# Kernel tuning notes

Measured on AMD Instinct MI355X. Metric: run time of the kernel, lower is better.

## Reference

```python
import jax, jax.numpy as jnp
import numpy as np

G, S, DG, HN, HE, L, F = 64, 160, 128, 128, 16, 2, 16


def _rn(k, shape, scale=0.05):
    return jax.random.normal(k, shape, dtype=jnp.float32) * scale


def setup_inputs() -> dict:
    ks = jax.random.split(jax.random.key(0), 26)
    return {
        "gene_codes": jax.random.normal(ks[0], (G, DG), dtype=jnp.float32),
        "node_entry_w": _rn(ks[1], (HN, DG)), "node_entry_b": _rn(ks[2], (HN,)),
        "node_wih0": _rn(ks[3], (4 * HN, 1)), "node_wih": _rn(ks[4], (L - 1, 4 * HN, HN)),
        "node_whh": _rn(ks[5], (L, 4 * HN, HN)), "node_bih": _rn(ks[6], (L, 4 * HN)), "node_bhh": _rn(ks[7], (L, 4 * HN)),
        "node_exit_w": _rn(ks[8], (32, HN)), "node_exit_b": _rn(ks[9], (32,)),
        "edge_entry_w": _rn(ks[10], (HE, 32)), "edge_entry_b": _rn(ks[11], (HE,)),
        "edge_wih0": _rn(ks[12], (4 * HE, 1)), "edge_wih": _rn(ks[13], (L - 1, 4 * HE, HE)),
        "edge_whh": _rn(ks[14], (L, 4 * HE, HE)), "edge_bih": _rn(ks[15], (L, 4 * HE)), "edge_bhh": _rn(ks[16], (L, 4 * HE)),
        "ee1_w": _rn(ks[17], (8, HE)), "ee1_b": _rn(ks[18], (8,)),
        "ee2_w": _rn(ks[19], (2, 8)), "ee2_b": _rn(ks[20], (2,)),
        "ef1_w": _rn(ks[21], (8, HE)), "ef1_b": _rn(ks[22], (8,)),
        "ef2_w": _rn(ks[23], (2 * F, 8)), "ef2_b": _rn(ks[24], (2 * F,)),
        "graphs_size": S,
    }


def _lstm_zero_input(h0, wih0, wih, whh, bih, bhh, steps):
    # Multi-layer PyTorch-style LSTM (gate order i,f,g,o) whose input sequence is all-zeros
    # of feature size 1; h0 is replicated across layers (as in the original .repeat).
    nl = whh.shape[0]
    h = jnp.stack([h0] * nl)
    c = jnp.zeros_like(h)
    zero_in = jnp.zeros((h0.shape[0], 1), h0.dtype)

    def step(carry, _):
        h, c = carry
        hs, cs = [], []
        inp = zero_in
        for l in range(nl):
            w_in = wih0 if l == 0 else wih[l - 1]
            gates = inp @ w_in.T + h[l] @ whh[l].T + bih[l] + bhh[l]
            i, f, g, o = jnp.split(gates, 4, axis=-1)
            cn = jax.nn.sigmoid(f) * c[l] + jax.nn.sigmoid(i) * jnp.tanh(g)
            hn = jax.nn.sigmoid(o) * jnp.tanh(cn)
            hs.append(hn); cs.append(cn)
            inp = hn
        return (jnp.stack(hs), jnp.stack(cs)), hs[-1]

    _, outs = jax.lax.scan(step, (h, c), None, length=steps)
    return outs  # [steps, B, H] top-layer hiddens


def reference(gene_codes, node_entry_w, node_entry_b, node_wih0, node_wih, node_whh, node_bih, node_bhh, node_exit_w, node_exit_b, edge_entry_w, edge_entry_b, edge_wih0, edge_wih, edge_whh, edge_bih, edge_bhh, ee1_w, ee1_b, ee2_w, ee2_b, ef1_w, ef1_b, ef2_w, ef2_b, graphs_size):
    s_len = int(graphs_size)
    g_n = gene_codes.shape[0]
    n_max = s_len + 1
    m = s_len * g_n  # total node steps == number of edge sequences
    fdim = ef2_w.shape[0] // 2

    # node RNN over zero inputs, h0 from gene codes
    h0n = jax.nn.relu(gene_codes @ node_entry_w.T + node_entry_b)
    node_out = _lstm_zero_input(h0n, node_wih0, node_wih, node_whh, node_bih, node_bhh, s_len)  # [S,G,HN]
    # uniform graph sizes: torch's flipped packed data == reversed step-major layout,
    # flat index k -> (step = S-1-k//G, graph = k%G)
    node_flat = jnp.flip(node_out, axis=0).reshape(m, -1)

    # edge RNN: one sequence per node step; zero inputs, so full-length run gives
    # identical hiddens at every valid packed step
    h0e = jax.nn.relu(jax.nn.relu(node_flat @ node_exit_w.T + node_exit_b) @ edge_entry_w.T + edge_entry_b)
    eh = _lstm_zero_input(h0e, edge_wih0, edge_wih, edge_whh, edge_bih, edge_bhh, s_len)  # [S,M,HE]

    e = jax.nn.sigmoid(jax.nn.relu(eh @ ee1_w.T + ee1_b) @ ee2_w.T + ee2_b)          # [S,M,2]
    f = (jax.nn.relu(eh @ ef1_w.T + ef1_b) @ ef2_w.T + ef2_b).reshape(s_len, m, 2, fdim)

    # ragged index construction: edge sequence k has row = edges_size[k] = S - k//G,
    # graph id = k%G, valid steps s < row, column = s
    k = jnp.arange(m)
    gid = k % g_n
    row = s_len - k // g_n
    s = jnp.arange(s_len)[:, None]
    mask = (s < row[None, :]).reshape(-1)
    gid2 = jnp.broadcast_to(gid[None, :], (s_len, m)).reshape(-1)
    row2 = jnp.broadcast_to(row[None, :], (s_len, m)).reshape(-1)
    col2 = jnp.broadcast_to(s, (s_len, m)).reshape(-1)

    el = jnp.where(mask, e[..., 0].reshape(-1), 0.0)
    eu = jnp.where(mask, e[..., 1].reshape(-1), 0.0)
    exist = jnp.zeros((g_n, n_max, n_max), gene_codes.dtype)
    exist = exist.at[gid2, row2, col2].add(el).at[gid2, col2, row2].add(eu)

    fl = jnp.where(mask[:, None], f[:, :, 0, :].reshape(-1, fdim), 0.0)
    fu = jnp.where(mask[:, None], f[:, :, 1, :].reshape(-1, fdim), 0.0)
    feat = jnp.zeros((g_n, n_max, n_max, fdim), gene_codes.dtype)
    feat = feat.at[gid2, row2, col2].add(fl).at[gid2, col2, row2].add(fu)
    return exist, feat
```

## Files before the change

### kernel.cpp

```cpp
#include <hip/hip_runtime.h>


typedef __attribute__((ext_vector_type(8))) short short8;
typedef __attribute__((ext_vector_type(4))) short short4v;
typedef __attribute__((ext_vector_type(4))) float floatx4;
typedef _Float16 half2v __attribute__((ext_vector_type(2)));

#define NG 64
#define NMAX 161

__device__ __forceinline__ float sgm(float x) {
  return __builtin_amdgcn_rcpf(1.0f + __expf(-x));
}
__device__ __forceinline__ float tanhf_(float x) {
  return 2.0f * __builtin_amdgcn_rcpf(1.0f + __expf(-2.0f * x)) - 1.0f;
}
__device__ __forceinline__ unsigned short f2b(float x) {
  union { float f; unsigned u; } v; v.f = x;
  unsigned r = v.u + 0x7fffu + ((v.u >> 16) & 1u);
  return (unsigned short)(r >> 16);
}
__device__ __forceinline__ float b2f(unsigned short h) {
  union { unsigned u; float f; } v; v.u = ((unsigned)h) << 16; return v.f;
}
__device__ __forceinline__ half2v pkh(float a, float b) {
  return __builtin_bit_cast(half2v, __builtin_amdgcn_cvt_pkrtz(a, b));
}

#define RORF(x, N) __builtin_bit_cast(float, __builtin_amdgcn_update_dpp(      \
    __builtin_bit_cast(int, (x)), __builtin_bit_cast(int, (x)),                \
    0x120 | (N), 0xF, 0xF, false))

__device__ __forceinline__ void rotpack(float h, half2v* out) {
  const float r1  = RORF(h, 1),  r2  = RORF(h, 2),  r3  = RORF(h, 3);
  const float r4  = RORF(h, 4),  r5  = RORF(h, 5),  r6  = RORF(h, 6);
  const float r7  = RORF(h, 7),  r8  = RORF(h, 8),  r9  = RORF(h, 9);
  const float r10 = RORF(h, 10), r11 = RORF(h, 11), r12 = RORF(h, 12);
  const float r13 = RORF(h, 13), r14 = RORF(h, 14), r15 = RORF(h, 15);
  out[0] = pkh(h,   r1);
  out[1] = pkh(r2,  r3);
  out[2] = pkh(r4,  r5);
  out[3] = pkh(r6,  r7);
  out[4] = pkh(r8,  r9);
  out[5] = pkh(r10, r11);
  out[6] = pkh(r12, r13);
  out[7] = pkh(r14, r15);
}

__global__ __launch_bounds__(512) void node_l0(
    const float* __restrict__ gene,
    const float* __restrict__ entw,
    const float* __restrict__ entb,
    const float* __restrict__ nwhh,
    const float* __restrict__ nbih,
    const float* __restrict__ nbhh,
    unsigned short* __restrict__ h0w,
    unsigned short* __restrict__ hinit)
{
  const int tid  = threadIdx.x;
  const int wv   = tid >> 6;
  const int lane = tid & 63;
  const int lo   = lane & 15;
  const int hi   = lane >> 4;
  const int u    = (wv << 4) | lo;
  const int nb   = blockIdx.x;

  __shared__ __align__(16) unsigned short hA0[2][16][136];

  short8 B0[4][4];
#pragma unroll
  for (int t = 0; t < 4; ++t) {
    const int n = t * 128 + u;
#pragma unroll
    for (int ks = 0; ks < 4; ++ks) {
      const float* src = nwhh + n * 128 + ks * 32 + hi * 8;
      short8 bfr;
#pragma unroll
      for (int jj = 0; jj < 8; ++jj) bfr[jj] = (short)f2b(src[jj]);
      B0[t][ks] = bfr;
    }
  }

  const float bi0 = nbih[u]       + nbhh[u];
  const float bf0 = nbih[128 + u] + nbhh[128 + u];
  const float bg0 = nbih[256 + u] + nbhh[256 + u];
  const float bo0 = nbih[384 + u] + nbhh[384 + u];

  {
    const int q  = tid >> 5;
    const int u4 = (tid & 31) * 4;
    const float* gc = gene + (nb * 16 + q) * 128;
    float acc[4] = { entb[u4], entb[u4 + 1], entb[u4 + 2], entb[u4 + 3] };
    for (int qq = 0; qq < 32; ++qq) {
      const float4 gv = *(const float4*)&gc[qq * 4];
#pragma unroll
      for (int r = 0; r < 4; ++r) {
        const float4 wv2 = *(const float4*)&entw[(u4 + r) * 128 + qq * 4];
        acc[r] += gv.x * wv2.x + gv.y * wv2.y + gv.z * wv2.z + gv.w * wv2.w;
      }
    }
#pragma unroll
    for (int r = 0; r < 4; ++r) {
      const unsigned short hb = f2b(fmaxf(acc[r], 0.0f));
      hA0[0][q][u4 + r] = hb;
      hinit[(size_t)(nb * 16 + q) * 128 + u4 + r] = hb;
    }
  }

  float c0[4] = {0.f, 0.f, 0.f, 0.f};
  __syncthreads();

  for (int t = 0; t < 160; ++t) {
    const int rb = t & 1, wb = rb ^ 1;
    floatx4 a0 = {bi0, bi0, bi0, bi0};
    floatx4 a1 = {bf0, bf0, bf0, bf0};
    floatx4 a2 = {bg0, bg0, bg0, bg0};
    floatx4 a3 = {bo0, bo0, bo0, bo0};
    const unsigned short* ar = &hA0[rb][lo][hi * 8];
#pragma unroll
    for (int ks = 0; ks < 4; ++ks) {
      const short8 afr = *(const short8*)(ar + ks * 32);
      a0 = __builtin_amdgcn_mfma_f32_16x16x32_bf16(afr, B0[0][ks], a0, 0, 0, 0);
      a1 = __builtin_amdgcn_mfma_f32_16x16x32_bf16(afr, B0[1][ks], a1, 0, 0, 0);
      a2 = __builtin_amdgcn_mfma_f32_16x16x32_bf16(afr, B0[2][ks], a2, 0, 0, 0);
      a3 = __builtin_amdgcn_mfma_f32_16x16x32_bf16(afr, B0[3][ks], a3, 0, 0, 0);
    }
    const size_t obase = (size_t)(t * 64 + nb * 16) * 128;
#pragma unroll
    for (int r = 0; r < 4; ++r) {
      const float iv = sgm(a0[r]);
      const float fv = sgm(a1[r]);
      const float gv = tanhf_(a2[r]);
      const float ov = sgm(a3[r]);
      const float cn = fv * c0[r] + iv * gv;
      c0[r] = cn;
      const unsigned short hb = f2b(ov * tanhf_(cn));
      const int q = hi * 4 + r;
      hA0[wb][q][u] = hb;
      h0w[obase + (size_t)q * 128 + u] = hb;
    }
    __syncthreads();
  }
}

__global__ __launch_bounds__(256) void xgemm(
    const unsigned short* __restrict__ h0w,
    const float* __restrict__ nwih,
    unsigned short* __restrict__ X3)
{
  const int tid = threadIdx.x;
  const int wv  = tid >> 6;
  const int lane = tid & 63;
  const int lo  = lane & 15;
  const int hi  = lane >> 4;
  const int bt  = blockIdx.x;
  const int bn  = blockIdx.y;

  __shared__ __align__(16) unsigned short s_b[128][136];

  for (int i = tid; i < 128 * 32; i += 256) {
    const int nc = i >> 5, k4 = (i & 31) * 4;
    const float4 w = *(const float4*)&nwih[(size_t)(bn * 128 + nc) * 128 + k4];
    s_b[nc][k4]     = f2b(w.x);
    s_b[nc][k4 + 1] = f2b(w.y);
    s_b[nc][k4 + 2] = f2b(w.z);
    s_b[nc][k4 + 3] = f2b(w.w);
  }
  __syncthreads();

  floatx4 acc[8];
#pragma unroll
  for (int nt = 0; nt < 8; ++nt) acc[nt] = (floatx4){0.f, 0.f, 0.f, 0.f};

  const unsigned short* arow = h0w + (size_t)(bt * 64 + wv * 16 + lo) * 128 + hi * 8;
#pragma unroll
  for (int ks = 0; ks < 4; ++ks) {
    const short8 afr = *(const short8*)(arow + ks * 32);
#pragma unroll
    for (int nt = 0; nt < 8; ++nt) {
      const short8 bfr = *(const short8*)&s_b[nt * 16 + lo][ks * 32 + hi * 8];
      acc[nt] = __builtin_amdgcn_mfma_f32_16x16x32_bf16(afr, bfr, acc[nt], 0, 0, 0);
    }
  }

#pragma unroll
  for (int nt = 0; nt < 8; ++nt) {
    const size_t base3 = ((((size_t)wv * 160 + bt) * 512) + bn * 128 + nt * 16 + lo) * 16 + hi * 4;
    short4v xv;
#pragma unroll
    for (int r = 0; r < 4; ++r) xv[r] = (short)f2b(acc[nt][r]);
    *(short4v*)&X3[base3] = xv;
  }
}

__global__ __launch_bounds__(512) void node_l1(
    const unsigned short* __restrict__ hinit,
    const unsigned short* __restrict__ X3,
    const float* __restrict__ nwhh,
    const float* __restrict__ nbih,
    const float* __restrict__ nbhh,
    unsigned short* __restrict__ nout)
{
  const int tid  = threadIdx.x;
  const int wv   = tid >> 6;
  const int lane = tid & 63;
  const int lo   = lane & 15;
  const int hi   = lane >> 4;
  const int u    = (wv << 4) | lo;
  const int nb   = blockIdx.x;

  __shared__ __align__(16) unsigned short hA1[2][16][136];

  short8 B1[4][4];
#pragma unroll
  for (int t = 0; t < 4; ++t) {
    const int n = t * 128 + u;
#pragma unroll
    for (int ks = 0; ks < 4; ++ks) {
      const float* src = nwhh + 512 * 128 + n * 128 + ks * 32 + hi * 8;
      short8 bfr;
#pragma unroll
      for (int jj = 0; jj < 8; ++jj) bfr[jj] = (short)f2b(src[jj]);
      B1[t][ks] = bfr;
    }
  }

  const float bi1 = nbih[512 + u]       + nbhh[512 + u];
  const float bf1 = nbih[512 + 128 + u] + nbhh[512 + 128 + u];
  const float bg1 = nbih[512 + 256 + u] + nbhh[512 + 256 + u];
  const float bo1 = nbih[512 + 384 + u] + nbhh[512 + 384 + u];

  {
    const int q  = tid >> 5;
    const int u4 = (tid & 31) * 4;
    const short4v hv = *(const short4v*)&hinit[(size_t)(nb * 16 + q) * 128 + u4];
    *(short4v*)&hA1[0][q][u4] = hv;
  }

  float c1[4] = {0.f, 0.f, 0.f, 0.f};

  const size_t xstep = 512 * 16;
  const unsigned short* xb = X3 + ((size_t)nb * 160) * xstep + (size_t)u * 16 + hi * 4;
  short4v x0 = *(const short4v*)(xb);
  short4v x1 = *(const short4v*)(xb + 128 * 16);
  short4v x2 = *(const short4v*)(xb + 256 * 16);
  short4v x3 = *(const short4v*)(xb + 384 * 16);
  __syncthreads();

  for (int t = 0; t < 160; ++t) {
    const int rb = t & 1, wb = rb ^ 1;

    floatx4 a0 = {bi1, bi1, bi1, bi1};
    floatx4 a1 = {bf1, bf1, bf1, bf1};
    floatx4 a2 = {bg1, bg1, bg1, bg1};
    floatx4 a3 = {bo1, bo1, bo1, bo1};
    const unsigned short* ar = &hA1[rb][lo][hi * 8];
#pragma unroll
    for (int ks = 0; ks < 4; ++ks) {
      const short8 afr = *(const short8*)(ar + ks * 32);
      a0 = __builtin_amdgcn_mfma_f32_16x16x32_bf16(afr, B1[0][ks], a0, 0, 0, 0);
      a1 = __builtin_amdgcn_mfma_f32_16x16x32_bf16(afr, B1[1][ks], a1, 0, 0, 0);
      a2 = __builtin_amdgcn_mfma_f32_16x16x32_bf16(afr, B1[2][ks], a2, 0, 0, 0);
      a3 = __builtin_amdgcn_mfma_f32_16x16x32_bf16(afr, B1[3][ks], a3, 0, 0, 0);
    }

    const short4v cx0 = x0, cx1 = x1, cx2 = x2, cx3 = x3;
    if (t + 1 < 160) {
      const unsigned short* xn = xb + (size_t)(t + 1) * xstep;
      x0 = *(const short4v*)(xn);
      x1 = *(const short4v*)(xn + 128 * 16);
      x2 = *(const short4v*)(xn + 256 * 16);
      x3 = *(const short4v*)(xn + 384 * 16);
    }

    const size_t obase = (size_t)((159 - t) * 64 + nb * 16) * 128;
#pragma unroll
    for (int r = 0; r < 4; ++r) {
      const float iv = sgm(a0[r] + b2f((unsigned short)cx0[r]));
      const float fv = sgm(a1[r] + b2f((unsigned short)cx1[r]));
      const float gv = tanhf_(a2[r] + b2f((unsigned short)cx2[r]));
      const float ov = sgm(a3[r] + b2f((unsigned short)cx3[r]));
      const float cn = fv * c1[r] + iv * gv;
      c1[r] = cn;
      const unsigned short hb = f2b(ov * tanhf_(cn));
      const int q = hi * 4 + r;
      hA1[wb][q][u] = hb;
      nout[obase + (size_t)q * 128 + u] = hb;
    }
    __syncthreads();
  }
}

__global__ __launch_bounds__(256, 1) void edge_kernel(
    const unsigned short* __restrict__ nflat,
    const float* __restrict__ exw, const float* __restrict__ exb,
    const float* __restrict__ enw, const float* __restrict__ enb,
    const float* __restrict__ ewih,
    const float* __restrict__ ewhh,
    const float* __restrict__ ebih, const float* __restrict__ ebhh,
    const float* __restrict__ ee1w, const float* __restrict__ ee1b,
    const float* __restrict__ ee2w, const float* __restrict__ ee2b,
    const float* __restrict__ ef1w, const float* __restrict__ ef1b,
    const float* __restrict__ ef2w, const float* __restrict__ ef2b,
    float* __restrict__ out)
{
  const int tid = threadIdx.x;
  const int sg  = tid >> 4;
  const int u   = tid & 15;
  const int b   = blockIdx.x;

  const int row = b >> 8, r = b & 255;
  const int bb  = (row == 1) ? (511 - r) : ((row << 8) + r);
  const int kbase = bb * 16;
  const int jrow  = 160 - (bb >> 2);
  const int gid   = (kbase & 63) + sg;

  __shared__ __align__(16) float s_nf[16][132];
  __shared__ float s_w0s[64][17];
  __shared__ float s_was[64][17];
  __shared__ float s_wbs[64][17];
  __shared__ float s_wh[16][17];
  __shared__ float s_ef2[32][10];
  __shared__ __align__(16) float s_ee2[16];
  __shared__ __align__(16) float t1b[16][12];
  __shared__ __align__(16) float t2b[16][12];
  __shared__ __align__(16) float x32[16][36];

  for (int i = tid; i < 16 * 128; i += 256)
    s_nf[i >> 7][i & 127] = b2f(nflat[(size_t)(kbase + (i >> 7)) * 128 + (i & 127)]);
  for (int i = tid; i < 64 * 16; i += 256) {
    s_w0s[i >> 4][i & 15] = ewhh[i];
    s_was[i >> 4][i & 15] = ewih[i];
    s_wbs[i >> 4][i & 15] = ewhh[1024 + i];
  }
  for (int i = tid; i < 8 * 16; i += 256) {
    s_wh[i >> 4][i & 15]       = ee1w[i];
    s_wh[8 + (i >> 4)][i & 15] = ef1w[i];
  }
  for (int i = tid; i < 32 * 8; i += 256) s_ef2[i >> 3][i & 7] = ef2w[i];
  if (tid < 16) s_ee2[tid] = ee2w[tid];

  if (b < NG) {
    for (int d = tid; d < NMAX; d += 256) {
      out[(size_t)b * (NMAX * NMAX) + (size_t)d * NMAX + d] = 0.0f;
      float* fb = out + (size_t)NG * NMAX * NMAX
                + ((size_t)b * NMAX * NMAX + (size_t)d * NMAX + d) * 16;
#pragma unroll
      for (int q = 0; q < 16; ++q) fb[q] = 0.0f;
    }
  }

  const float be0i = ebih[u]      + ebhh[u];
  const float be0f = ebih[16 + u] + ebhh[16 + u];
  const float be0g = ebih[32 + u] + ebhh[32 + u];
  const float be0o = ebih[48 + u] + ebhh[48 + u];
  const float be1i = ebih[64 + u]      + ebhh[64 + u];
  const float be1f = ebih[64 + 16 + u] + ebhh[64 + 16 + u];
  const float be1g = ebih[64 + 32 + u] + ebhh[64 + 32 + u];
  const float be1o = ebih[64 + 48 + u] + ebhh[64 + 48 + u];
  const float hbias = (u < 8) ? ee1b[u] : ef1b[u - 8];
  const float f2bl = ef2b[u], f2bu = ef2b[16 + u];
  const float e2bias = (u < 2) ? ee2b[u] : 0.0f;

  __syncthreads();

  half2v W0h[4][8], WAh[4][8], WBh[4][8], WHh[8];
#pragma unroll
  for (int g = 0; g < 4; ++g) {
    const int rw = g * 16 + u;
#pragma unroll
    for (int j = 0; j < 8; ++j) {
      const int v0 = (u + 2 * j) & 15, v1 = (u + 2 * j + 1) & 15;
      W0h[g][j] = pkh(s_w0s[rw][v0], s_w0s[rw][v1]);
      WAh[g][j] = pkh(s_was[rw][v0], s_was[rw][v1]);
      WBh[g][j] = pkh(s_wbs[rw][v0], s_wbs[rw][v1]);
    }
  }
#pragma unroll
  for (int j = 0; j < 8; ++j) {
    const int v0 = (u + 2 * j) & 15, v1 = (u + 2 * j + 1) & 15;
    WHh[j] = pkh(s_wh[u][v0], s_wh[u][v1]);
  }

  {
    float acc0 = exb[u], acc1 = exb[16 + u];
    const float* w0p = exw + u * 128;
    const float* w1p = exw + (16 + u) * 128;
    for (int qq = 0; qq < 32; ++qq) {
      const float4 nv  = *(const float4*)&s_nf[sg][qq * 4];
      const float4 w0v = *(const float4*)&w0p[qq * 4];
      const float4 w1v = *(const float4*)&w1p[qq * 4];
      acc0 += nv.x * w0v.x + nv.y * w0v.y + nv.z * w0v.z + nv.w * w0v.w;
      acc1 += nv.x * w1v.x + nv.y * w1v.y + nv.z * w1v.z + nv.w * w1v.w;
    }
    x32[sg][u] = fmaxf(acc0, 0.0f);
    x32[sg][16 + u] = fmaxf(acc1, 0.0f);
  }
  __builtin_amdgcn_wave_barrier();
  float c0 = 0.0f, c1 = 0.0f;
  half2v h20[8], h21[8];
  {
    float acc = enb[u];
    const float* ewp = enw + u * 32;
#pragma unroll
    for (int qq = 0; qq < 8; ++qq) {
      const float4 xv  = *(const float4*)&x32[sg][qq * 4];
      const float4 wv2 = *(const float4*)&ewp[qq * 4];
      acc += xv.x * wv2.x + xv.y * wv2.y + xv.z * wv2.z + xv.w * wv2.w;
    }
    const float h0e = fmaxf(acc, 0.0f);
    rotpack(h0e, h20);
#pragma unroll
    for (int j = 0; j < 8; ++j) h21[j] = h20[j];
  }

  float* exi = out + (size_t)gid * (NMAX * NMAX);
  float* fea = out + (size_t)NG * NMAX * NMAX + (size_t)gid * (NMAX * NMAX) * 16;
  const int jN = jrow * NMAX;

  for (int s = 0; s <= jrow; ++s) {
    const bool doStep = (s < jrow);
    const bool doHead = (s > 0);

    float a0, a1, a2, a3;
    if (doStep) {
      a0 = be0i; a1 = be0f; a2 = be0g; a3 = be0o;
#pragma unroll
      for (int j = 0; j < 8; ++j) {
        a0 = __builtin_amdgcn_fdot2(h20[j], W0h[0][j], a0, false);
        a1 = __builtin_amdgcn_fdot2(h20[j], W0h[1][j], a1, false);
        a2 = __builtin_amdgcn_fdot2(h20[j], W0h[2][j], a2, false);
        a3 = __builtin_amdgcn_fdot2(h20[j], W0h[3][j], a3, false);
      }
    }

    if (doHead) {
      __builtin_amdgcn_wave_barrier();
      const int sm = s - 1;
      const float2 ta0 = *(const float2*)&t2b[sg][0];
      const float2 ta1 = *(const float2*)&t2b[sg][2];
      const float2 ta2 = *(const float2*)&t2b[sg][4];
      const float2 ta3 = *(const float2*)&t2b[sg][6];
      const float2 wl0 = *(const float2*)&s_ef2[u][0];
      const float2 wl1 = *(const float2*)&s_ef2[u][2];
      const float2 wl2 = *(const float2*)&s_ef2[u][4];
      const float2 wl3 = *(const float2*)&s_ef2[u][6];
      const float2 wu0 = *(const float2*)&s_ef2[16 + u][0];
      const float2 wu1 = *(const float2*)&s_ef2[16 + u][2];
      const float2 wu2 = *(const float2*)&s_ef2[16 + u][4];
      const float2 wu3 = *(const float2*)&s_ef2[16 + u][6];
      const float fl = f2bl
          + ta0.x * wl0.x + ta0.y * wl0.y + ta1.x * wl1.x + ta1.y * wl1.y
          + ta2.x * wl2.x + ta2.y * wl2.y + ta3.x * wl3.x + ta3.y * wl3.y;
      const float fu = f2bu
          + ta0.x * wu0.x + ta0.y * wu0.y + ta1.x * wu1.x + ta1.y * wu1.y
          + ta2.x * wu2.x + ta2.y * wu2.y + ta3.x * wu3.x + ta3.y * wu3.y;
      fea[((size_t)jN + sm) * 16 + u] = fl;
      fea[((size_t)sm * NMAX + jrow) * 16 + u] = fu;
      if (u < 2) {
        const float4 t1a = *(const float4*)&t1b[sg][0];
        const float4 t1c = *(const float4*)&t1b[sg][4];
        const float4 we0 = *(const float4*)&s_ee2[u * 8];
        const float4 we1 = *(const float4*)&s_ee2[u * 8 + 4];
        float e = e2bias
            + t1a.x * we0.x + t1a.y * we0.y + t1a.z * we0.z + t1a.w * we0.w
            + t1c.x * we1.x + t1c.y * we1.y + t1c.z * we1.z + t1c.w * we1.w;
        const size_t idx = (u == 0) ? ((size_t)jN + sm)
                                    : ((size_t)sm * NMAX + jrow);
        exi[idx] = sgm(e);
      }
    }

    if (doStep) {
      {
        const float iv = sgm(a0), fv = sgm(a1), gv = tanhf_(a2), ov = sgm(a3);
        c0 = fv * c0 + iv * gv;
        rotpack(ov * tanhf_(c0), h20);
      }
      float b0 = be1i, b1 = be1f, b2 = be1g, b3 = be1o;
#pragma unroll
      for (int j = 0; j < 8; ++j) {
        b0 = __builtin_amdgcn_fdot2(h20[j], WAh[0][j], b0, false);
        b1 = __builtin_amdgcn_fdot2(h20[j], WAh[1][j], b1, false);
        b2 = __builtin_amdgcn_fdot2(h20[j], WAh[2][j], b2, false);
        b3 = __builtin_amdgcn_fdot2(h20[j], WAh[3][j], b3, false);
      }
#pragma unroll
      for (int j = 0; j < 8; ++j) {
        b0 = __builtin_amdgcn_fdot2(h21[j], WBh[0][j], b0, false);
        b1 = __builtin_amdgcn_fdot2(h21[j], WBh[1][j], b1, false);
        b2 = __builtin_amdgcn_fdot2(h21[j], WBh[2][j], b2, false);
        b3 = __builtin_amdgcn_fdot2(h21[j], WBh[3][j], b3, false);
      }
      {
        const float iv = sgm(b0), fv = sgm(b1), gv = tanhf_(b2), ov = sgm(b3);
        c1 = fv * c1 + iv * gv;
        rotpack(ov * tanhf_(c1), h21);
      }
      {
        float th = hbias;
#pragma unroll
        for (int j = 0; j < 8; ++j)
          th = __builtin_amdgcn_fdot2(h21[j], WHh[j], th, false);
        th = fmaxf(th, 0.0f);
        if (u < 8) t1b[sg][u] = th; else t2b[sg][u - 8] = th;
      }
      __builtin_amdgcn_wave_barrier();
    }
  }
}

extern "C" void kernel_launch(void* const* d_in, const int* in_sizes, int n_in,
                              void* d_out, int out_size, void* d_ws, size_t ws_size,
                              hipStream_t stream) {
  (void)in_sizes; (void)n_in; (void)out_size; (void)ws_size;
  const float* gene = (const float*)d_in[0];
  const float* entw = (const float*)d_in[1];
  const float* entb = (const float*)d_in[2];
  const float* nwih = (const float*)d_in[4];
  const float* nwhh = (const float*)d_in[5];
  const float* nbih = (const float*)d_in[6];
  const float* nbhh = (const float*)d_in[7];
  const float* exw  = (const float*)d_in[8];
  const float* exb  = (const float*)d_in[9];
  const float* enw  = (const float*)d_in[10];
  const float* enb  = (const float*)d_in[11];
  const float* ewih = (const float*)d_in[13];
  const float* ewhh = (const float*)d_in[14];
  const float* ebih = (const float*)d_in[15];
  const float* ebhh = (const float*)d_in[16];
  const float* ee1w = (const float*)d_in[17];
  const float* ee1b = (const float*)d_in[18];
  const float* ee2w = (const float*)d_in[19];
  const float* ee2b = (const float*)d_in[20];
  const float* ef1w = (const float*)d_in[21];
  const float* ef1b = (const float*)d_in[22];
  const float* ef2w = (const float*)d_in[23];
  const float* ef2b = (const float*)d_in[24];

  char* ws = (char*)d_ws;
  unsigned short* nflat = (unsigned short*)(ws);
  unsigned short* h0w   = (unsigned short*)(ws + 2621440);
  unsigned short* hinit = (unsigned short*)(ws + 5242880);
  unsigned short* X3    = (unsigned short*)(ws + 5259264);

  node_l0<<<4, 512, 0, stream>>>(gene, entw, entb, nwhh, nbih, nbhh, h0w, hinit);
  xgemm<<<dim3(160, 4), 256, 0, stream>>>(h0w, nwih, X3);
  node_l1<<<4, 512, 0, stream>>>(hinit, X3, nwhh, nbih, nbhh, nflat);
  edge_kernel<<<640, 256, 0, stream>>>(nflat, exw, exb, enw, enb, ewih, ewhh,
                                       ebih, ebhh, ee1w, ee1b, ee2w, ee2b,
                                       ef1w, ef1b, ef2w, ef2b, (float*)d_out);
}
```

Before: 501.6 us.

## Fuse node LSTM layers and input GEMM into one flag-pipelined persistent kernel

Replaces the three sequential node kernels (layer-0 recurrence, input-projection GEMM, layer-1 recurrence) with one 12-block launch. Blocks take three roles and hand work along through per-timestep global atomic flags, so the layer-1 recurrence can run one step behind layer 0 instead of waiting for it to finish. The initial hidden state is recomputed in the layer-1 blocks rather than stored and reloaded, and outputs use nontemporal stores. It adds spin-wait and fence latency on every step and relies on all 12 blocks being resident at the same time, and the layer-1 loop loses its one-step X prefetch.

```diff
diff --git a/kernel.cpp b/kernel.cpp
--- a/kernel.cpp
+++ b/kernel.cpp
@@ -47,247 +47,255 @@
   out[7] = pkh(r14, r15);
 }
 
-__global__ __launch_bounds__(512) void node_l0(
+__global__ __launch_bounds__(512) void node_fused(
     const float* __restrict__ gene,
     const float* __restrict__ entw,
     const float* __restrict__ entb,
+    const float* __restrict__ nwih,
     const float* __restrict__ nwhh,
     const float* __restrict__ nbih,
     const float* __restrict__ nbhh,
     unsigned short* __restrict__ h0w,
-    unsigned short* __restrict__ hinit)
+    unsigned short* __restrict__ X3,
+    unsigned short* __restrict__ nflat,
+    int* __restrict__ flag0, int* __restrict__ flag1)
 {
+  __shared__ __align__(16) unsigned short hA[2][16][136];
+  __shared__ __align__(16) unsigned short s_b[128][136];
+
   const int tid  = threadIdx.x;
+  const int role = blockIdx.x >> 2;
+  const int rb4  = blockIdx.x & 3;
   const int wv   = tid >> 6;
   const int lane = tid & 63;
   const int lo   = lane & 15;
   const int hi   = lane >> 4;
-  const int u    = (wv << 4) | lo;
-  const int nb   = blockIdx.x;
-
-  __shared__ __align__(16) unsigned short hA0[2][16][136];
-
-  short8 B0[4][4];
-#pragma unroll
-  for (int t = 0; t < 4; ++t) {
-    const int n = t * 128 + u;
-#pragma unroll
-    for (int ks = 0; ks < 4; ++ks) {
-      const float* src = nwhh + n * 128 + ks * 32 + hi * 8;
-      short8 bfr;
-#pragma unroll
-      for (int jj = 0; jj < 8; ++jj) bfr[jj] = (short)f2b(src[jj]);
-      B0[t][ks] = bfr;
-    }
-  }
-
-  const float bi0 = nbih[u]       + nbhh[u];
-  const float bf0 = nbih[128 + u] + nbhh[128 + u];
-  const float bg0 = nbih[256 + u] + nbhh[256 + u];
-  const float bo0 = nbih[384 + u] + nbhh[384 + u];
-
-  {
-    const int q  = tid >> 5;
-    const int u4 = (tid & 31) * 4;
-    const float* gc = gene + (nb * 16 + q) * 128;
-    float acc[4] = { entb[u4], entb[u4 + 1], entb[u4 + 2], entb[u4 + 3] };
-    for (int qq = 0; qq < 32; ++qq) {
-      const float4 gv = *(const float4*)&gc[qq * 4];
+
+  if (role == 0) {
+    const int nb = rb4;
+    const int u  = (wv << 4) | lo;
+
+    short8 B0[4][4];
+#pragma unroll
+    for (int t = 0; t < 4; ++t) {
+      const int n = t * 128 + u;
+#pragma unroll
+      for (int ks = 0; ks < 4; ++ks) {
+        const float* src = nwhh + n * 128 + ks * 32 + hi * 8;
+        short8 bfr;
+#pragma unroll
+        for (int jj = 0; jj < 8; ++jj) bfr[jj] = (short)f2b(src[jj]);
+        B0[t][ks] = bfr;
+      }
+    }
+    const float bi0 = nbih[u]       + nbhh[u];
+    const float bf0 = nbih[128 + u] + nbhh[128 + u];
+    const float bg0 = nbih[256 + u] + nbhh[256 + u];
+    const float bo0 = nbih[384 + u] + nbhh[384 + u];
+
+    {
+      const int q  = tid >> 5;
+      const int u4 = (tid & 31) * 4;
+      const float* gc = gene + (nb * 16 + q) * 128;
+      float acc[4] = { entb[u4], entb[u4 + 1], entb[u4 + 2], entb[u4 + 3] };
+      for (int qq = 0; qq < 32; ++qq) {
+        const float4 gv = *(const float4*)&gc[qq * 4];
+#pragma unroll
+        for (int r = 0; r < 4; ++r) {
+          const float4 wv2 = *(const float4*)&entw[(u4 + r) * 128 + qq * 4];
+          acc[r] += gv.x * wv2.x + gv.y * wv2.y + gv.z * wv2.z + gv.w * wv2.w;
+        }
+      }
+#pragma unroll
+      for (int r = 0; r < 4; ++r)
+        hA[0][q][u4 + r] = f2b(fmaxf(acc[r], 0.0f));
+    }
+
+    float c0[4] = {0.f, 0.f, 0.f, 0.f};
+    for (int t = 0; t < 160; ++t) {
+      __syncthreads();
+      if (t > 0 && tid == 0) {
+        __threadfence();
+        __hip_atomic_fetch_add(&flag0[t - 1], 1, __ATOMIC_RELEASE,
+                               __HIP_MEMORY_SCOPE_AGENT);
+      }
+      const int rb = t & 1, wb = rb ^ 1;
+      floatx4 a0 = {bi0, bi0, bi0, bi0};
+      floatx4 a1 = {bf0, bf0, bf0, bf0};
+      floatx4 a2 = {bg0, bg0, bg0, bg0};
+      floatx4 a3 = {bo0, bo0, bo0, bo0};
+      const unsigned short* ar = &hA[rb][lo][hi * 8];
+#pragma unroll
+      for (int ks = 0; ks < 4; ++ks) {
+        const short8 afr = *(const short8*)(ar + ks * 32);
+        a0 = __builtin_amdgcn_mfma_f32_16x16x32_bf16(afr, B0[0][ks], a0, 0, 0, 0);
+        a1 = __builtin_amdgcn_mfma_f32_16x16x32_bf16(afr, B0[1][ks], a1, 0, 0, 0);
+        a2 = __builtin_amdgcn_mfma_f32_16x16x32_bf16(afr, B0[2][ks], a2, 0, 0, 0);
+        a3 = __builtin_amdgcn_mfma_f32_16x16x32_bf16(afr, B0[3][ks], a3, 0, 0, 0);
+      }
+      const size_t obase = (size_t)(t * 64 + nb * 16) * 128;
 #pragma unroll
       for (int r = 0; r < 4; ++r) {
-        const float4 wv2 = *(const float4*)&entw[(u4 + r) * 128 + qq * 4];
-        acc[r] += gv.x * wv2.x + gv.y * wv2.y + gv.z * wv2.z + gv.w * wv2.w;
-      }
-    }
-#pragma unroll
-    for (int r = 0; r < 4; ++r) {
-      const unsigned short hb = f2b(fmaxf(acc[r], 0.0f));
-      hA0[0][q][u4 + r] = hb;
-      hinit[(size_t)(nb * 16 + q) * 128 + u4 + r] = hb;
-    }
-  }
-
-  float c0[4] = {0.f, 0.f, 0.f, 0.f};
-  __syncthreads();
-
-  for (int t = 0; t < 160; ++t) {
-    const int rb = t & 1, wb = rb ^ 1;
-    floatx4 a0 = {bi0, bi0, bi0, bi0};
-    floatx4 a1 = {bf0, bf0, bf0, bf0};
-    floatx4 a2 = {bg0, bg0, bg0, bg0};
-    floatx4 a3 = {bo0, bo0, bo0, bo0};
-    const unsigned short* ar = &hA0[rb][lo][hi * 8];
-#pragma unroll
-    for (int ks = 0; ks < 4; ++ks) {
-      const short8 afr = *(const short8*)(ar + ks * 32);
-      a0 = __builtin_amdgcn_mfma_f32_16x16x32_bf16(afr, B0[0][ks], a0, 0, 0, 0);
-      a1 = __builtin_amdgcn_mfma_f32_16x16x32_bf16(afr, B0[1][ks], a1, 0, 0, 0);
-      a2 = __builtin_amdgcn_mfma_f32_16x16x32_bf16(afr, B0[2][ks], a2, 0, 0, 0);
-      a3 = __builtin_amdgcn_mfma_f32_16x16x32_bf16(afr, B0[3][ks], a3, 0, 0, 0);
-    }
-    const size_t obase = (size_t)(t * 64 + nb * 16) * 128;
-#pragma unroll
-    for (int r = 0; r < 4; ++r) {
-      const float iv = sgm(a0[r]);
-      const float fv = sgm(a1[r]);
-      const float gv = tanhf_(a2[r]);
-      const float ov = sgm(a3[r]);
-      const float cn = fv * c0[r] + iv * gv;
-      c0[r] = cn;
-      const unsigned short hb = f2b(ov * tanhf_(cn));
-      const int q = hi * 4 + r;
-      hA0[wb][q][u] = hb;
-      h0w[obase + (size_t)q * 128 + u] = hb;
+        const float iv = sgm(a0[r]);
+        const float fv = sgm(a1[r]);
+        const float gv = tanhf_(a2[r]);
+        const float ov = sgm(a3[r]);
+        const float cn = fv * c0[r] + iv * gv;
+        c0[r] = cn;
+        const unsigned short hb = f2b(ov * tanhf_(cn));
+        const int q = hi * 4 + r;
+        hA[wb][q][u] = hb;
+        __builtin_nontemporal_store(hb, &h0w[obase + (size_t)q * 128 + u]);
+      }
     }
     __syncthreads();
-  }
-}
-
-__global__ __launch_bounds__(256) void xgemm(
-    const unsigned short* __restrict__ h0w,
-    const float* __restrict__ nwih,
-    unsigned short* __restrict__ X3)
-{
-  const int tid = threadIdx.x;
-  const int wv  = tid >> 6;
-  const int lane = tid & 63;
-  const int lo  = lane & 15;
-  const int hi  = lane >> 4;
-  const int bt  = blockIdx.x;
-  const int bn  = blockIdx.y;
-
-  __shared__ __align__(16) unsigned short s_b[128][136];
-
-  for (int i = tid; i < 128 * 32; i += 256) {
-    const int nc = i >> 5, k4 = (i & 31) * 4;
-    const float4 w = *(const float4*)&nwih[(size_t)(bn * 128 + nc) * 128 + k4];
-    s_b[nc][k4]     = f2b(w.x);
-    s_b[nc][k4 + 1] = f2b(w.y);
-    s_b[nc][k4 + 2] = f2b(w.z);
-    s_b[nc][k4 + 3] = f2b(w.w);
-  }
-  __syncthreads();
-
-  floatx4 acc[8];
-#pragma unroll
-  for (int nt = 0; nt < 8; ++nt) acc[nt] = (floatx4){0.f, 0.f, 0.f, 0.f};
-
-  const unsigned short* arow = h0w + (size_t)(bt * 64 + wv * 16 + lo) * 128 + hi * 8;
-#pragma unroll
-  for (int ks = 0; ks < 4; ++ks) {
-    const short8 afr = *(const short8*)(arow + ks * 32);
-#pragma unroll
-    for (int nt = 0; nt < 8; ++nt) {
-      const short8 bfr = *(const short8*)&s_b[nt * 16 + lo][ks * 32 + hi * 8];
-      acc[nt] = __builtin_amdgcn_mfma_f32_16x16x32_bf16(afr, bfr, acc[nt], 0, 0, 0);
-    }
-  }
-
-#pragma unroll
-  for (int nt = 0; nt < 8; ++nt) {
-    const size_t base3 = ((((size_t)wv * 160 + bt) * 512) + bn * 128 + nt * 16 + lo) * 16 + hi * 4;
-    short4v xv;
-#pragma unroll
-    for (int r = 0; r < 4; ++r) xv[r] = (short)f2b(acc[nt][r]);
-    *(short4v*)&X3[base3] = xv;
-  }
-}
-
-__global__ __launch_bounds__(512) void node_l1(
-    const unsigned short* __restrict__ hinit,
-    const unsigned short* __restrict__ X3,
-    const float* __restrict__ nwhh,
-    const float* __restrict__ nbih,
-    const float* __restrict__ nbhh,
-    unsigned short* __restrict__ nout)
-{
-  const int tid  = threadIdx.x;
-  const int wv   = tid >> 6;
-  const int lane = tid & 63;
-  const int lo   = lane & 15;
-  const int hi   = lane >> 4;
-  const int u    = (wv << 4) | lo;
-  const int nb   = blockIdx.x;
-
-  __shared__ __align__(16) unsigned short hA1[2][16][136];
-
-  short8 B1[4][4];
-#pragma unroll
-  for (int t = 0; t < 4; ++t) {
-    const int n = t * 128 + u;
-#pragma unroll
-    for (int ks = 0; ks < 4; ++ks) {
-      const float* src = nwhh + 512 * 128 + n * 128 + ks * 32 + hi * 8;
-      short8 bfr;
-#pragma unroll
-      for (int jj = 0; jj < 8; ++jj) bfr[jj] = (short)f2b(src[jj]);
-      B1[t][ks] = bfr;
-    }
-  }
-
-  const float bi1 = nbih[512 + u]       + nbhh[512 + u];
-  const float bf1 = nbih[512 + 128 + u] + nbhh[512 + 128 + u];
-  const float bg1 = nbih[512 + 256 + u] + nbhh[512 + 256 + u];
-  const float bo1 = nbih[512 + 384 + u] + nbhh[512 + 384 + u];
-
-  {
-    const int q  = tid >> 5;
-    const int u4 = (tid & 31) * 4;
-    const short4v hv = *(const short4v*)&hinit[(size_t)(nb * 16 + q) * 128 + u4];
-    *(short4v*)&hA1[0][q][u4] = hv;
-  }
-
-  float c1[4] = {0.f, 0.f, 0.f, 0.f};
-
-  const size_t xstep = 512 * 16;
-  const unsigned short* xb = X3 + ((size_t)nb * 160) * xstep + (size_t)u * 16 + hi * 4;
-  short4v x0 = *(const short4v*)(xb);
-  short4v x1 = *(const short4v*)(xb + 128 * 16);
-  short4v x2 = *(const short4v*)(xb + 256 * 16);
-  short4v x3 = *(const short4v*)(xb + 384 * 16);
-  __syncthreads();
-
-  for (int t = 0; t < 160; ++t) {
-    const int rb = t & 1, wb = rb ^ 1;
-
-    floatx4 a0 = {bi1, bi1, bi1, bi1};
-    floatx4 a1 = {bf1, bf1, bf1, bf1};
-    floatx4 a2 = {bg1, bg1, bg1, bg1};
-    floatx4 a3 = {bo1, bo1, bo1, bo1};
-    const unsigned short* ar = &hA1[rb][lo][hi * 8];
-#pragma unroll
-    for (int ks = 0; ks < 4; ++ks) {
-      const short8 afr = *(const short8*)(ar + ks * 32);
-      a0 = __builtin_amdgcn_mfma_f32_16x16x32_bf16(afr, B1[0][ks], a0, 0, 0, 0);
-      a1 = __builtin_amdgcn_mfma_f32_16x16x32_bf16(afr, B1[1][ks], a1, 0, 0, 0);
-      a2 = __builtin_amdgcn_mfma_f32_16x16x32_bf16(afr, B1[2][ks], a2, 0, 0, 0);
-      a3 = __builtin_amdgcn_mfma_f32_16x16x32_bf16(afr, B1[3][ks], a3, 0, 0, 0);
-    }
-
-    const short4v cx0 = x0, cx1 = x1, cx2 = x2, cx3 = x3;
-    if (t + 1 < 160) {
-      const unsigned short* xn = xb + (size_t)(t + 1) * xstep;
-      x0 = *(const short4v*)(xn);
-      x1 = *(const short4v*)(xn + 128 * 16);
-      x2 = *(const short4v*)(xn + 256 * 16);
-      x3 = *(const short4v*)(xn + 384 * 16);
-    }
-
-    const size_t obase = (size_t)((159 - t) * 64 + nb * 16) * 128;
-#pragma unroll
-    for (int r = 0; r < 4; ++r) {
-      const float iv = sgm(a0[r] + b2f((unsigned short)cx0[r]));
-      const float fv = sgm(a1[r] + b2f((unsigned short)cx1[r]));
-      const float gv = tanhf_(a2[r] + b2f((unsigned short)cx2[r]));
-      const float ov = sgm(a3[r] + b2f((unsigned short)cx3[r]));
-      const float cn = fv * c1[r] + iv * gv;
-      c1[r] = cn;
-      const unsigned short hb = f2b(ov * tanhf_(cn));
-      const int q = hi * 4 + r;
-      hA1[wb][q][u] = hb;
-      nout[obase + (size_t)q * 128 + u] = hb;
-    }
-    __syncthreads();
+    if (tid == 0) {
+      __threadfence();
+      __hip_atomic_fetch_add(&flag0[159], 1, __ATOMIC_RELEASE,
+                             __HIP_MEMORY_SCOPE_AGENT);
+    }
+
+  } else if (role == 1) {
+    const int xg = rb4;
+    for (int i = tid; i < 128 * 32; i += 512) {
+      const int nc = i >> 5, k4 = (i & 31) * 4;
+      const float4 w = *(const float4*)&nwih[(size_t)(xg * 128 + nc) * 128 + k4];
+      s_b[nc][k4]     = f2b(w.x);
+      s_b[nc][k4 + 1] = f2b(w.y);
+      s_b[nc][k4 + 2] = f2b(w.z);
+      s_b[nc][k4 + 3] = f2b(w.w);
+    }
+    const int gg = wv & 3;
+    const int ch = wv >> 2;
+
+    for (int t = 0; t < 160; ++t) {
+      if (tid == 0) {
+        while (__hip_atomic_load(&flag0[t], __ATOMIC_ACQUIRE,
+                                 __HIP_MEMORY_SCOPE_AGENT) < 4)
+          __builtin_amdgcn_s_sleep(2);
+        __threadfence();
+      }
+      __syncthreads();
+
+      floatx4 acc[4];
+#pragma unroll
+      for (int nt = 0; nt < 4; ++nt) acc[nt] = (floatx4){0.f, 0.f, 0.f, 0.f};
+      const unsigned short* arow =
+          h0w + (size_t)(t * 64 + gg * 16 + lo) * 128 + hi * 8;
+#pragma unroll
+      for (int ks = 0; ks < 4; ++ks) {
+        const short8 afr = *(const short8*)(arow + ks * 32);
+#pragma unroll
+        for (int nt = 0; nt < 4; ++nt) {
+          const short8 bfr =
+              *(const short8*)&s_b[ch * 64 + nt * 16 + lo][ks * 32 + hi * 8];
+          acc[nt] = __builtin_amdgcn_mfma_f32_16x16x32_bf16(afr, bfr, acc[nt], 0, 0, 0);
+        }
+      }
+#pragma unroll
+      for (int nt = 0; nt < 4; ++nt) {
+        const size_t base3 =
+            ((((size_t)gg * 160 + t) * 512) + xg * 128 + ch * 64 + nt * 16 + lo) * 16
+            + hi * 4;
+        short4v xv;
+#pragma unroll
+        for (int r = 0; r < 4; ++r) xv[r] = (short)f2b(acc[nt][r]);
+        __builtin_nontemporal_store(xv, (short4v*)&X3[base3]);
+      }
+      __syncthreads();
+      if (tid == 0) {
+        __threadfence();
+        __hip_atomic_fetch_add(&flag1[t], 1, __ATOMIC_RELEASE,
+                               __HIP_MEMORY_SCOPE_AGENT);
+      }
+    }
+
+  } else {
+    const int nb = rb4;
+    const int u  = (wv << 4) | lo;
+
+    short8 B1[4][4];
+#pragma unroll
+    for (int t = 0; t < 4; ++t) {
+      const int n = t * 128 + u;
+#pragma unroll
+      for (int ks = 0; ks < 4; ++ks) {
+        const float* src = nwhh + 512 * 128 + n * 128 + ks * 32 + hi * 8;
+        short8 bfr;
+#pragma unroll
+        for (int jj = 0; jj < 8; ++jj) bfr[jj] = (short)f2b(src[jj]);
+        B1[t][ks] = bfr;
+      }
+    }
+    const float bi1 = nbih[512 + u]       + nbhh[512 + u];
+    const float bf1 = nbih[512 + 128 + u] + nbhh[512 + 128 + u];
+    const float bg1 = nbih[512 + 256 + u] + nbhh[512 + 256 + u];
+    const float bo1 = nbih[512 + 384 + u] + nbhh[512 + 384 + u];
+
+    {
+      const int q  = tid >> 5;
+      const int u4 = (tid & 31) * 4;
+      const float* gc = gene + (nb * 16 + q) * 128;
+      float acc[4] = { entb[u4], entb[u4 + 1], entb[u4 + 2], entb[u4 + 3] };
+      for (int qq = 0; qq < 32; ++qq) {
+        const float4 gv = *(const float4*)&gc[qq * 4];
+#pragma unroll
+        for (int r = 0; r < 4; ++r) {
+          const float4 wv2 = *(const float4*)&entw[(u4 + r) * 128 + qq * 4];
+          acc[r] += gv.x * wv2.x + gv.y * wv2.y + gv.z * wv2.z + gv.w * wv2.w;
+        }
+      }
+#pragma unroll
+      for (int r = 0; r < 4; ++r)
+        hA[0][q][u4 + r] = f2b(fmaxf(acc[r], 0.0f));
+    }
+
+    float c1[4] = {0.f, 0.f, 0.f, 0.f};
+    for (int t = 0; t < 160; ++t) {
+      if (tid == 0) {
+        while (__hip_atomic_load(&flag1[t], __ATOMIC_ACQUIRE,
+                                 __HIP_MEMORY_SCOPE_AGENT) < 4)
+          __builtin_amdgcn_s_sleep(2);
+        __threadfence();
+      }
+      __syncthreads();
+
+      const int rb = t & 1, wb = rb ^ 1;
+      const unsigned short* xp =
+          X3 + ((size_t)(nb * 160 + t)) * (512 * 16) + (size_t)u * 16 + hi * 4;
+      const short4v x0 = *(const short4v*)(xp);
+      const short4v x1 = *(const short4v*)(xp + 128 * 16);
+      const short4v x2 = *(const short4v*)(xp + 256 * 16);
+      const short4v x3 = *(const short4v*)(xp + 384 * 16);
+
+      floatx4 a0 = {bi1, bi1, bi1, bi1};
+      floatx4 a1 = {bf1, bf1, bf1, bf1};
+      floatx4 a2 = {bg1, bg1, bg1, bg1};
+      floatx4 a3 = {bo1, bo1, bo1, bo1};
+      const unsigned short* ar = &hA[rb][lo][hi * 8];
+#pragma unroll
+      for (int ks = 0; ks < 4; ++ks) {
+        const short8 afr = *(const short8*)(ar + ks * 32);
+        a0 = __builtin_amdgcn_mfma_f32_16x16x32_bf16(afr, B1[0][ks], a0, 0, 0, 0);
+        a1 = __builtin_amdgcn_mfma_f32_16x16x32_bf16(afr, B1[1][ks], a1, 0, 0, 0);
+        a2 = __builtin_amdgcn_mfma_f32_16x16x32_bf16(afr, B1[2][ks], a2, 0, 0, 0);
+        a3 = __builtin_amdgcn_mfma_f32_16x16x32_bf16(afr, B1[3][ks], a3, 0, 0, 0);
+      }
+      const size_t obase = (size_t)((159 - t) * 64 + nb * 16) * 128;
+#pragma unroll
+      for (int r = 0; r < 4; ++r) {
+        const float iv = sgm(a0[r] + b2f((unsigned short)x0[r]));
+        const float fv = sgm(a1[r] + b2f((unsigned short)x1[r]));
+        const float gv = tanhf_(a2[r] + b2f((unsigned short)x2[r]));
+        const float ov = sgm(a3[r] + b2f((unsigned short)x3[r]));
+        const float cn = fv * c1[r] + iv * gv;
+        c1[r] = cn;
+        const unsigned short hb = f2b(ov * tanhf_(cn));
+        const int q = hi * 4 + r;
+        hA[wb][q][u] = hb;
+        __builtin_nontemporal_store(hb, &nflat[obase + (size_t)q * 128 + u]);
+      }
+    }
   }
 }
 
@@ -541,12 +549,13 @@
   char* ws = (char*)d_ws;
   unsigned short* nflat = (unsigned short*)(ws);
   unsigned short* h0w   = (unsigned short*)(ws + 2621440);
-  unsigned short* hinit = (unsigned short*)(ws + 5242880);
+  int* flag0            = (int*)(ws + 5242880);
+  int* flag1            = (int*)(ws + 5242880 + 4096);
   unsigned short* X3    = (unsigned short*)(ws + 5259264);
 
-  node_l0<<<4, 512, 0, stream>>>(gene, entw, entb, nwhh, nbih, nbhh, h0w, hinit);
-  xgemm<<<dim3(160, 4), 256, 0, stream>>>(h0w, nwih, X3);
-  node_l1<<<4, 512, 0, stream>>>(hinit, X3, nwhh, nbih, nbhh, nflat);
+  hipMemsetAsync(ws + 5242880, 0, 8192, stream);
+  node_fused<<<12, 512, 0, stream>>>(gene, entw, entb, nwih, nwhh, nbih, nbhh,
+                                     h0w, X3, nflat, flag0, flag1);
   edge_kernel<<<640, 256, 0, stream>>>(nflat, exw, exb, enw, enb, ewih, ewhh,
                                        ebih, ebhh, ee1w, ee1b, ee2w, ee2b,
                                        ef1w, ef1b, ef2w, ef2b, (float*)d_out);
```

After: 655.4 us, median of 2. +30.7%, slower.
